# Kernel optimization log

Measured on AMD Instinct MI355X. Metric: run time of the kernel, lower is better.

The kernel has to match this reference:

```python
import jax, jax.numpy as jnp
import numpy as np
import math

EMBED_DIM = 1024
NUM_HEADS = 16
HEAD_DIM = EMBED_DIM // NUM_HEADS
ROPE_BASE = 10000.0


def _rope_cache(seq_len, dim, dtype=jnp.float32):
    inv_freq = 1.0 / (ROPE_BASE ** (jnp.arange(0, dim, 2, dtype=jnp.float32) / dim))
    t = jnp.arange(seq_len, dtype=jnp.float32)
    freqs = t[:, None] * inv_freq[None, :]          # [S, D/2]
    emb = jnp.concatenate([freqs, freqs], axis=-1)  # [S, D]
    return jnp.cos(emb).astype(dtype), jnp.sin(emb).astype(dtype)


def _rotate_half(x):
    x1, x2 = jnp.split(x, 2, axis=-1)
    return jnp.concatenate([-x2, x1], axis=-1)


def setup_inputs() -> dict:
    key = jax.random.key(0)
    ks = jax.random.split(key, 12)
    B, S, E = 2, 2048, EMBED_DIM
    s = 1.0 / math.sqrt(E)
    inp = {
        "query": jax.random.normal(ks[0], (B, S, E), jnp.float32),
        "key": jax.random.normal(ks[1], (B, S, E), jnp.float32),
        "value": jax.random.normal(ks[2], (B, S, E), jnp.float32),
        "Wq": jax.random.normal(ks[3], (E, E), jnp.float32) * s,
        "bq": jnp.zeros((E,), jnp.float32),
        "Wk": jax.random.normal(ks[4], (E, E), jnp.float32) * s,
        "bk": jnp.zeros((E,), jnp.float32),
        "Wv": jax.random.normal(ks[5], (E, E), jnp.float32) * s,
        "bv": jnp.zeros((E,), jnp.float32),
        "Wo": jax.random.normal(ks[6], (E, E), jnp.float32) * s,
        "bo": jnp.zeros((E,), jnp.float32),
    }
    return inp


def reference(query, key, value, Wq, bq, Wk, bk, Wv, bv, Wo, bo):
    B, S, E = query.shape
    H, D = NUM_HEADS, HEAD_DIM

    def proj(x, W, b):  # torch Linear: x @ W.T + b -> [B,H,S,D]
        return (x @ W.T + b).reshape(B, -1, H, D).transpose(0, 2, 1, 3)

    q = proj(query, Wq, bq)
    k = proj(key, Wk, bk)
    v = proj(value, Wv, bv)

    cos, sin = _rope_cache(S, D, q.dtype)  # [S, D]
    cos = cos[None, None]                  # [1,1,S,D]
    sin = sin[None, None]
    q = q * cos + _rotate_half(q) * sin
    k = k * cos + _rotate_half(k) * sin

    scale = 1.0 / math.sqrt(D)
    scores = jnp.einsum("bhsd,bhtd->bhst", q, k) * scale  # [B,H,S,S]
    causal = jnp.triu(jnp.ones((S, S), bool), k=1)
    scores = jnp.where(causal[None, None], -jnp.inf, scores)
    attn = jax.nn.softmax(scores, axis=-1)
    out = jnp.einsum("bhst,bhtd->bhsd", attn, v)           # [B,H,S,D]
    out = out.transpose(0, 2, 1, 3).reshape(B, S, E)
    return out @ Wo.T + bo
```

## Files before the change

### kernel.cpp

```cpp
#include <hip/hip_runtime.h>
#include <math.h>

typedef unsigned short u16;
typedef __attribute__((ext_vector_type(4))) float f32x4;
typedef __attribute__((ext_vector_type(8))) short bf16x8;

#define SEQ   2048
#define EMB   1024
#define NH    16
#define HD    64
#define MROWS 4096

__device__ __forceinline__ u16 f2b(float f) {
    unsigned u = __float_as_uint(f);
    u += 0x7fff + ((u >> 16) & 1);
    return (u16)(u >> 16);
}
__device__ __forceinline__ unsigned pack_bf16x2(float a, float b) {
    unsigned ua = __float_as_uint(a) + 0x8000u;
    unsigned ub = __float_as_uint(b) + 0x8000u;
    return __builtin_amdgcn_perm(ub, ua, 0x07060302u);
}
__device__ __forceinline__ void gld16(const u16* g, const u16* l) {
    __builtin_amdgcn_global_load_lds((const __attribute__((address_space(1))) void*)g,
                                     (__attribute__((address_space(3))) void*)l, 16, 0, 0);
}

__global__ void k_f2b3(const float* __restrict__ s0, const float* __restrict__ s1,
                       const float* __restrict__ s2, u16* d0, u16* d1, u16* d2, int n8) {
    const float* src = (blockIdx.z == 0) ? s0 : (blockIdx.z == 1 ? s1 : s2);
    u16* dst = (blockIdx.z == 0) ? d0 : (blockIdx.z == 1 ? d1 : d2);
    int i = blockIdx.x * blockDim.x + threadIdx.x;
    if (i >= n8) return;
    const float4* s4 = (const float4*)src;
    float4 a = s4[i * 2], b = s4[i * 2 + 1];
    union { u16 u[8]; uint4 v; } o;
    o.u[0] = f2b(a.x); o.u[1] = f2b(a.y); o.u[2] = f2b(a.z); o.u[3] = f2b(a.w);
    o.u[4] = f2b(b.x); o.u[5] = f2b(b.y); o.u[6] = f2b(b.z); o.u[7] = f2b(b.w);
    ((uint4*)dst)[i] = o.v;
}
__global__ void k_f2b4(const float* __restrict__ s0, const float* __restrict__ s1,
                       const float* __restrict__ s2, const float* __restrict__ s3,
                       u16* d0, u16* d1, u16* d2, u16* d3, int n8) {
    const float* src = (blockIdx.z == 0) ? s0 : (blockIdx.z == 1 ? s1 : (blockIdx.z == 2 ? s2 : s3));
    u16* dst = (blockIdx.z == 0) ? d0 : (blockIdx.z == 1 ? d1 : (blockIdx.z == 2 ? d2 : d3));
    int i = blockIdx.x * blockDim.x + threadIdx.x;
    if (i >= n8) return;
    const float4* s4 = (const float4*)src;
    float4 a = s4[i * 2], b = s4[i * 2 + 1];
    union { u16 u[8]; uint4 v; } o;
    o.u[0] = f2b(a.x); o.u[1] = f2b(a.y); o.u[2] = f2b(a.z); o.u[3] = f2b(a.w);
    o.u[4] = f2b(b.x); o.u[5] = f2b(b.y); o.u[6] = f2b(b.z); o.u[7] = f2b(b.w);
    ((uint4*)dst)[i] = o.v;
}

struct GemmArgs {
    const u16* A; const u16* Bw; const float* bias; u16* Cb;
};

__global__ __launch_bounds__(256) void k_gemm_qkv(GemmArgs g0, GemmArgs g1, GemmArgs g2) {
    GemmArgs g = (blockIdx.z == 0) ? g0 : (blockIdx.z == 1 ? g1 : g2);
    __shared__ union {
        u16 s[2][8192];
        u16 tr[4][4608];
    } sh;

    int tid = threadIdx.x;
    int wave = tid >> 6, lane = tid & 63, quad = lane >> 4, l16 = lane & 15;
    int wm = wave >> 1, wn = wave & 1;
    int m0 = blockIdx.y * 128, n0 = blockIdx.x * 128;
    const int K = EMB;

    auto stage = [&](int k0, u16* buf) {
#pragma unroll
        for (int pp = 0; pp < 4; pp++) {
            int slot = pp * 256 + tid;
            int p = slot & 3;
            const u16* gsrc;
            if (pp < 2) {
                int row = slot >> 2;
                int c = p ^ (row & 3);
                gsrc = g.A + (size_t)(m0 + row) * K + k0 + c * 8;
            } else {
                int row = (slot >> 2) - 128;
                int c = p ^ (row & 3);
                gsrc = g.Bw + (size_t)(n0 + row) * K + k0 + c * 8;
            }
            gld16(gsrc, buf + slot * 8);
        }
    };

    f32x4 acc[4][4];
#pragma unroll
    for (int i = 0; i < 4; i++)
#pragma unroll
        for (int j = 0; j < 4; j++) acc[i][j] = (f32x4){0.f, 0.f, 0.f, 0.f};

    int nk = K >> 5;
    stage(0, sh.s[0]);
    for (int ks = 0; ks < nk; ks++) {
        __syncthreads();
        if (ks + 1 < nk) stage((ks + 1) << 5, sh.s[(ks + 1) & 1]);
        const u16* Ab = sh.s[ks & 1];
        const u16* Bb = Ab + 4096;
        bf16x8 af[4], bfr[4];
#pragma unroll
        for (int i = 0; i < 4; i++) {
            int row = wm * 64 + i * 16 + l16;
            af[i] = *(const bf16x8*)&Ab[row * 32 + (quad ^ (row & 3)) * 8];
        }
#pragma unroll
        for (int j = 0; j < 4; j++) {
            int row = wn * 64 + j * 16 + l16;
            bfr[j] = *(const bf16x8*)&Bb[row * 32 + (quad ^ (row & 3)) * 8];
        }
#pragma unroll
        for (int i = 0; i < 4; i++)
#pragma unroll
            for (int j = 0; j < 4; j++)
                acc[i][j] = __builtin_amdgcn_mfma_f32_16x16x32_bf16(af[i], bfr[j], acc[i][j], 0, 0, 0);
    }

    if (blockIdx.z < 2) {
        float qscale = (blockIdx.z == 0) ? 0.18033688011112042f : 1.0f;
#pragma unroll
        for (int j = 0; j < 2; j++) {
            int col1 = n0 + wn * 64 + j * 16 + l16;
            int dd1 = col1 & 63;
            int h = col1 >> 6;
            float inv = __expf(-(float)dd1 * 0.28782313662425575f);
            float b1 = g.bias[col1], b2 = g.bias[col1 + 32];
#pragma unroll
            for (int i = 0; i < 4; i++)
#pragma unroll
                for (int r = 0; r < 4; r++) {
                    int row = m0 + wm * 64 + i * 16 + quad * 4 + r;
                    int b = row >> 11, s = row & (SEQ - 1);
                    float sn, cs;
                    __sincosf((float)s * inv, &sn, &cs);
                    float x1 = acc[i][j][r] + b1;
                    float x2 = acc[i][j + 2][r] + b2;
                    size_t base = ((size_t)(b * NH + h) * SEQ + s) << 6;
                    g.Cb[base + dd1]      = f2b((x1 * cs - x2 * sn) * qscale);
                    g.Cb[base + dd1 + 32] = f2b((x2 * cs + x1 * sn) * qscale);
                }
        }
    } else {
        __syncthreads();
        u16* tr = sh.tr[wave];
        int h = (n0 >> 6) + wn;
        int b = m0 >> 11;
        int s0 = (m0 & (SEQ - 1)) + wm * 64;
#pragma unroll
        for (int j = 0; j < 4; j++) {
            float bv = g.bias[n0 + wn * 64 + j * 16 + l16];
#pragma unroll
            for (int i = 0; i < 4; i++) {
                uint2 pk;
                pk.x = pack_bf16x2(acc[i][j][0] + bv, acc[i][j][1] + bv);
                pk.y = pack_bf16x2(acc[i][j][2] + bv, acc[i][j][3] + bv);
                *(uint2*)&tr[(j * 16 + l16) * 72 + i * 16 + quad * 4] = pk;
            }
        }
        u16* dst = g.Cb + (((size_t)(b * NH + h) * HD) * SEQ) + s0;
#pragma unroll
        for (int ps = 0; ps < 8; ps++) {
            int d = ps * 8 + (lane >> 3);
            int sl = (lane & 7) * 8;
            uint4 v = *(const uint4*)&tr[d * 72 + sl];
            *(uint4*)&dst[(size_t)d * SEQ + sl] = v;
        }
    }
}

__global__ __launch_bounds__(256) void k_gemm_o(const u16* __restrict__ A,
                                                const u16* __restrict__ Bw,
                                                const float* __restrict__ bias,
                                                float* __restrict__ C) {
    __shared__ u16 sb[2][6144];
    int tid = threadIdx.x;
    int w = tid >> 6, lane = tid & 63, quad = lane >> 4, l16 = lane & 15;
    int m0 = blockIdx.y * 64, n0 = blockIdx.x * 128;
    const int K = EMB;

    auto stage = [&](int k0, u16* buf) {
#pragma unroll
        for (int pp = 0; pp < 3; pp++) {
            int slot = pp * 256 + tid;
            if (slot < 256) {
                int row = slot >> 2, p = slot & 3;
                int c = p ^ (row & 3);
                gld16(A + (size_t)(m0 + row) * K + k0 + c * 8, buf + slot * 8);
            } else {
                int s2 = slot - 256;
                int row = s2 >> 2, p = s2 & 3;
                int c = p ^ (row & 3);
                gld16(Bw + (size_t)(n0 + row) * K + k0 + c * 8, buf + 2048 + s2 * 8);
            }
        }
    };

    f32x4 acc[4][2];
#pragma unroll
    for (int i = 0; i < 4; i++)
#pragma unroll
        for (int j = 0; j < 2; j++) acc[i][j] = (f32x4){0.f, 0.f, 0.f, 0.f};

    int nk = K >> 5;
    stage(0, sb[0]);
    for (int ks = 0; ks < nk; ks++) {
        __syncthreads();
        if (ks + 1 < nk) stage((ks + 1) << 5, sb[(ks + 1) & 1]);
        const u16* Ab = sb[ks & 1];
        const u16* Bb = Ab + 2048;
        bf16x8 af[4], bf[2];
#pragma unroll
        for (int i = 0; i < 4; i++) {
            int row = i * 16 + l16;
            af[i] = *(const bf16x8*)&Ab[row * 32 + (quad ^ (row & 3)) * 8];
        }
#pragma unroll
        for (int j = 0; j < 2; j++) {
            int row = w * 32 + j * 16 + l16;
            bf[j] = *(const bf16x8*)&Bb[row * 32 + (quad ^ (row & 3)) * 8];
        }
#pragma unroll
        for (int i = 0; i < 4; i++)
#pragma unroll
            for (int j = 0; j < 2; j++)
                acc[i][j] = __builtin_amdgcn_mfma_f32_16x16x32_bf16(af[i], bf[j], acc[i][j], 0, 0, 0);
    }

#pragma unroll
    for (int i = 0; i < 4; i++)
#pragma unroll
        for (int r = 0; r < 4; r++) {
            int row = m0 + i * 16 + quad * 4 + r;
#pragma unroll
            for (int j = 0; j < 2; j++) {
                int col = n0 + w * 32 + j * 16 + l16;
                C[(size_t)row * EMB + col] = acc[i][j][r] + bias[col];
            }
        }
}

__global__ __launch_bounds__(256, 2) void k_attn(const u16* __restrict__ Q,
                                                 const u16* __restrict__ K,
                                                 const u16* __restrict__ Vt,
                                                 u16* __restrict__ O) {
    __shared__ u16 sbuf[2][8192];
    __shared__ u16 Pl[4][2048];
    int tid = threadIdx.x;
    int w = tid >> 6, lane = tid & 63, quad = lane >> 4, l16 = lane & 15;
    int bh = blockIdx.x & 31;
    int qt = 15 - (blockIdx.x >> 5);
    int q0w = qt * 128 + w * 32;

    const u16* Qb = Q + (size_t)bh * SEQ * HD;
    const u16* Kb = K + (size_t)bh * SEQ * HD;
    const u16* Vb = Vt + (size_t)bh * HD * SEQ;
    u16* pl = Pl[w];

    auto stage = [&](int t0, u16* buf) {
#pragma unroll
        for (int pp = 0; pp < 4; pp++) {
            int slot = pp * 256 + tid;
            int r = (slot >> 3) & 63;
            int p = slot & 7;
            int c = p ^ (r & 7);
            const u16* gsrc = (pp < 2) ? Kb + (size_t)(t0 + r) * HD + c * 8
                                       : Vb + (size_t)r * SEQ + t0 + c * 8;
            gld16(gsrc, buf + slot * 8);
        }
    };

    bf16x8 bq[2][2];
#pragma unroll
    for (int g = 0; g < 2; g++) {
        size_t base = (size_t)(q0w + g * 16 + l16) * HD + quad * 8;
        bq[g][0] = *(const bf16x8*)&Qb[base];
        bq[g][1] = *(const bf16x8*)&Qb[base + 32];
    }

    f32x4 o2[2][4];
#pragma unroll
    for (int g = 0; g < 2; g++)
#pragma unroll
        for (int jd = 0; jd < 4; jd++) o2[g][jd] = (f32x4){0.f, 0.f, 0.f, 0.f};
    float l_p[2] = {0.f, 0.f};

    int niter = 2 * qt + 2;
    stage(0, sbuf[0]);
    for (int it = 0; it < niter; ++it) {
        __syncthreads();
        if (it + 1 < niter) stage((it + 1) * 64, sbuf[(it + 1) & 1]);
        const u16* Kl = sbuf[it & 1];
        const u16* Vl = Kl + 4096;
        int t0 = it * 64;

        bf16x8 kf[4][2], vf[4][2];
#pragma unroll
        for (int mt = 0; mt < 4; mt++) {
            int row = mt * 16 + l16;
            kf[mt][0] = *(const bf16x8*)&Kl[row * 64 + (quad ^ (row & 7)) * 8];
            kf[mt][1] = *(const bf16x8*)&Kl[row * 64 + ((quad + 4) ^ (row & 7)) * 8];
            vf[mt][0] = *(const bf16x8*)&Vl[row * 64 + (quad ^ (row & 7)) * 8];
            vf[mt][1] = *(const bf16x8*)&Vl[row * 64 + ((quad + 4) ^ (row & 7)) * 8];
        }

#pragma unroll
        for (int g = 0; g < 2; g++) {
            int qmin = q0w + g * 16;
            if (t0 > qmin + 15) continue;

            f32x4 sc[4];
#pragma unroll
            for (int mt = 0; mt < 4; mt++) {
                sc[mt] = (f32x4){0.f, 0.f, 0.f, 0.f};
                sc[mt] = __builtin_amdgcn_mfma_f32_16x16x32_bf16(kf[mt][0], bq[g][0], sc[mt], 0, 0, 0);
                sc[mt] = __builtin_amdgcn_mfma_f32_16x16x32_bf16(kf[mt][1], bq[g][1], sc[mt], 0, 0, 0);
            }

            if (t0 + 63 > qmin) {
                int q = qmin + l16;
#pragma unroll
                for (int mt = 0; mt < 4; mt++)
#pragma unroll
                    for (int r = 0; r < 4; r++) {
                        int t = t0 + mt * 16 + quad * 4 + r;
                        if (t > q) sc[mt][r] = -INFINITY;
                    }
            }

            float rs = 0.f;
#pragma unroll
            for (int mt = 0; mt < 4; mt++)
#pragma unroll
                for (int r = 0; r < 4; r++) {
                    float p = __builtin_amdgcn_exp2f(sc[mt][r] - 64.f);
                    sc[mt][r] = p;
                    rs += p;
                }
            l_p[g] += rs;

            u16* plg = pl + g * 1024;
#pragma unroll
            for (int mt = 0; mt < 4; mt++) {
                uint2 pk;
                pk.x = pack_bf16x2(sc[mt][0], sc[mt][1]);
                pk.y = pack_bf16x2(sc[mt][2], sc[mt][3]);
                int chunk = 2 * mt + (quad >> 1);
                *(uint2*)&plg[l16 * 64 + (chunk ^ (l16 & 7)) * 8 + (quad & 1) * 4] = pk;
            }

            bf16x8 pb0 = *(const bf16x8*)&plg[l16 * 64 + (quad ^ (l16 & 7)) * 8];
            bf16x8 pb1 = *(const bf16x8*)&plg[l16 * 64 + ((quad + 4) ^ (l16 & 7)) * 8];

#pragma unroll
            for (int jd = 0; jd < 4; jd++) {
                o2[g][jd] = __builtin_amdgcn_mfma_f32_16x16x32_bf16(vf[jd][0], pb0, o2[g][jd], 0, 0, 0);
                o2[g][jd] = __builtin_amdgcn_mfma_f32_16x16x32_bf16(vf[jd][1], pb1, o2[g][jd], 0, 0, 0);
            }
        }
    }

    int b = bh >> 4, h = bh & (NH - 1);
#pragma unroll
    for (int g = 0; g < 2; g++) {
        float l = l_p[g];
        l += __shfl_xor(l, 16, 64);
        l += __shfl_xor(l, 32, 64);
        float inv = 1.f / l;
#pragma unroll
        for (int jd = 0; jd < 4; jd++) {
            uint2 pk;
            pk.x = pack_bf16x2(o2[g][jd][0] * inv, o2[g][jd][1] * inv);
            pk.y = pack_bf16x2(o2[g][jd][2] * inv, o2[g][jd][3] * inv);
            *(uint2*)&pl[l16 * 72 + jd * 16 + quad * 4] = pk;
        }
        int row = lane >> 2, dc = (lane & 3) * 16;
        uint4 d0 = *(const uint4*)&pl[row * 72 + dc];
        uint4 d1 = *(const uint4*)&pl[row * 72 + dc + 8];
        int q = q0w + g * 16 + row;
        size_t addr = (size_t)(b * SEQ + q) * EMB + h * HD + dc;
        *(uint4*)&O[addr] = d0;
        *(uint4*)&O[addr + 8] = d1;
    }
}

extern "C" void kernel_launch(void* const* d_in, const int* in_sizes, int n_in,
                              void* d_out, int out_size, void* d_ws, size_t ws_size,
                              hipStream_t stream) {
    const float* query = (const float*)d_in[0];
    const float* key_  = (const float*)d_in[1];
    const float* value = (const float*)d_in[2];
    const float* Wq = (const float*)d_in[3];
    const float* bq = (const float*)d_in[4];
    const float* Wk = (const float*)d_in[5];
    const float* bk = (const float*)d_in[6];
    const float* Wv = (const float*)d_in[7];
    const float* bv = (const float*)d_in[8];
    const float* Wo = (const float*)d_in[9];
    const float* bo = (const float*)d_in[10];
    float* out = (float*)d_out;

    char* ws = (char*)d_ws;
    const size_t MB = 1u << 20;
    u16* xq  = (u16*)(ws + 0 * MB);
    u16* xk  = (u16*)(ws + 8 * MB);
    u16* xv  = (u16*)(ws + 16 * MB);
    u16* wqb = (u16*)(ws + 24 * MB);
    u16* wkb = (u16*)(ws + 26 * MB);
    u16* wvb = (u16*)(ws + 28 * MB);
    u16* wob = (u16*)(ws + 30 * MB);
    u16* Qp  = (u16*)(ws + 32 * MB);
    u16* Kp  = (u16*)(ws + 40 * MB);
    u16* Vt  = (u16*)(ws + 48 * MB);
    u16* Ab  = xk;

    const int NX = MROWS * EMB;
    const int NW = EMB * EMB;

    k_f2b3<<<dim3(NX / (256 * 8), 1, 3), 256, 0, stream>>>(query, key_, value, xq, xk, xv, NX / 8);
    k_f2b4<<<dim3(NW / (256 * 8), 1, 4), 256, 0, stream>>>(Wq, Wk, Wv, Wo, wqb, wkb, wvb, wob, NW / 8);

    GemmArgs gq = { xq, wqb, bq, Qp };
    GemmArgs gk = { xk, wkb, bk, Kp };
    GemmArgs gv = { xv, wvb, bv, Vt };
    k_gemm_qkv<<<dim3(EMB / 128, MROWS / 128, 3), 256, 0, stream>>>(gq, gk, gv);

    k_attn<<<512, 256, 0, stream>>>(Qp, Kp, Vt, Ab);

    k_gemm_o<<<dim3(EMB / 128, MROWS / 64), 256, 0, stream>>>(Ab, wob, bo, out);
}
```

Before: 225.3 us.

## Merge conversion launches, remap GEMM block order, swizzle V-transpose shared buffer

After: 216.5 us. -3.9%, faster.

```diff
diff --git a/kernel.cpp b/kernel.cpp
--- a/kernel.cpp
+++ b/kernel.cpp
@@ -26,31 +26,27 @@
                                      (__attribute__((address_space(3))) void*)l, 16, 0, 0);
 }
 
-__global__ void k_f2b3(const float* __restrict__ s0, const float* __restrict__ s1,
-                       const float* __restrict__ s2, u16* d0, u16* d1, u16* d2, int n8) {
-    const float* src = (blockIdx.z == 0) ? s0 : (blockIdx.z == 1 ? s1 : s2);
-    u16* dst = (blockIdx.z == 0) ? d0 : (blockIdx.z == 1 ? d1 : d2);
-    int i = blockIdx.x * blockDim.x + threadIdx.x;
-    if (i >= n8) return;
+struct F2BArgs { const float* s[7]; u16* d[7]; };
+
+__global__ void k_f2b(F2BArgs a) {
+    int id = blockIdx.x;
+    const float* src; u16* dst; int base;
+    if (id < 6144) {
+        int z = id >> 11;
+        src = a.s[z]; dst = a.d[z];
+        base = (id & 2047) << 8;
+    } else {
+        int r = id - 6144;
+        int z = 3 + (r >> 9);
+        src = a.s[z]; dst = a.d[z];
+        base = (r & 511) << 8;
+    }
+    int i = base + threadIdx.x;
     const float4* s4 = (const float4*)src;
-    float4 a = s4[i * 2], b = s4[i * 2 + 1];
+    float4 x = s4[i * 2], y = s4[i * 2 + 1];
     union { u16 u[8]; uint4 v; } o;
-    o.u[0] = f2b(a.x); o.u[1] = f2b(a.y); o.u[2] = f2b(a.z); o.u[3] = f2b(a.w);
-    o.u[4] = f2b(b.x); o.u[5] = f2b(b.y); o.u[6] = f2b(b.z); o.u[7] = f2b(b.w);
-    ((uint4*)dst)[i] = o.v;
-}
-__global__ void k_f2b4(const float* __restrict__ s0, const float* __restrict__ s1,
-                       const float* __restrict__ s2, const float* __restrict__ s3,
-                       u16* d0, u16* d1, u16* d2, u16* d3, int n8) {
-    const float* src = (blockIdx.z == 0) ? s0 : (blockIdx.z == 1 ? s1 : (blockIdx.z == 2 ? s2 : s3));
-    u16* dst = (blockIdx.z == 0) ? d0 : (blockIdx.z == 1 ? d1 : (blockIdx.z == 2 ? d2 : d3));
-    int i = blockIdx.x * blockDim.x + threadIdx.x;
-    if (i >= n8) return;
-    const float4* s4 = (const float4*)src;
-    float4 a = s4[i * 2], b = s4[i * 2 + 1];
-    union { u16 u[8]; uint4 v; } o;
-    o.u[0] = f2b(a.x); o.u[1] = f2b(a.y); o.u[2] = f2b(a.z); o.u[3] = f2b(a.w);
-    o.u[4] = f2b(b.x); o.u[5] = f2b(b.y); o.u[6] = f2b(b.z); o.u[7] = f2b(b.w);
+    o.u[0] = f2b(x.x); o.u[1] = f2b(x.y); o.u[2] = f2b(x.z); o.u[3] = f2b(x.w);
+    o.u[4] = f2b(y.x); o.u[5] = f2b(y.y); o.u[6] = f2b(y.z); o.u[7] = f2b(y.w);
     ((uint4*)dst)[i] = o.v;
 }
 
@@ -59,16 +55,19 @@
 };
 
 __global__ __launch_bounds__(256) void k_gemm_qkv(GemmArgs g0, GemmArgs g1, GemmArgs g2) {
-    GemmArgs g = (blockIdx.z == 0) ? g0 : (blockIdx.z == 1 ? g1 : g2);
-    __shared__ union {
-        u16 s[2][8192];
-        u16 tr[4][4608];
-    } sh;
+    __shared__ u16 sbuf[2][8192];
+
+    int id = blockIdx.x;
+    int x = id / 96;
+    int rem = id % 96;
+    int z = rem >> 5;
+    int y = rem & 31;
+    GemmArgs g = (z == 0) ? g0 : (z == 1 ? g1 : g2);
 
     int tid = threadIdx.x;
     int wave = tid >> 6, lane = tid & 63, quad = lane >> 4, l16 = lane & 15;
     int wm = wave >> 1, wn = wave & 1;
-    int m0 = blockIdx.y * 128, n0 = blockIdx.x * 128;
+    int m0 = y * 128, n0 = x * 128;
     const int K = EMB;
 
     auto stage = [&](int k0, u16* buf) {
@@ -97,11 +96,11 @@
         for (int j = 0; j < 4; j++) acc[i][j] = (f32x4){0.f, 0.f, 0.f, 0.f};
 
     int nk = K >> 5;
-    stage(0, sh.s[0]);
+    stage(0, sbuf[0]);
     for (int ks = 0; ks < nk; ks++) {
         __syncthreads();
-        if (ks + 1 < nk) stage((ks + 1) << 5, sh.s[(ks + 1) & 1]);
-        const u16* Ab = sh.s[ks & 1];
+        if (ks + 1 < nk) stage((ks + 1) << 5, sbuf[(ks + 1) & 1]);
+        const u16* Ab = sbuf[ks & 1];
         const u16* Bb = Ab + 4096;
         bf16x8 af[4], bfr[4];
 #pragma unroll
@@ -121,8 +120,8 @@
                 acc[i][j] = __builtin_amdgcn_mfma_f32_16x16x32_bf16(af[i], bfr[j], acc[i][j], 0, 0, 0);
     }
 
-    if (blockIdx.z < 2) {
-        float qscale = (blockIdx.z == 0) ? 0.18033688011112042f : 1.0f;
+    if (z < 2) {
+        float qscale = (z == 0) ? 0.18033688011112042f : 1.0f;
 #pragma unroll
         for (int j = 0; j < 2; j++) {
             int col1 = n0 + wn * 64 + j * 16 + l16;
@@ -147,7 +146,7 @@
         }
     } else {
         __syncthreads();
-        u16* tr = sh.tr[wave];
+        u16* tr = &sbuf[0][0] + wave * 4096;
         int h = (n0 >> 6) + wn;
         int b = m0 >> 11;
         int s0 = (m0 & (SEQ - 1)) + wm * 64;
@@ -159,16 +158,18 @@
                 uint2 pk;
                 pk.x = pack_bf16x2(acc[i][j][0] + bv, acc[i][j][1] + bv);
                 pk.y = pack_bf16x2(acc[i][j][2] + bv, acc[i][j][3] + bv);
-                *(uint2*)&tr[(j * 16 + l16) * 72 + i * 16 + quad * 4] = pk;
+                int row = j * 16 + l16;
+                int c4 = i * 4 + quad;
+                *(uint2*)&tr[row * 64 + ((c4 ^ (row & 14)) << 2)] = pk;
             }
         }
         u16* dst = g.Cb + (((size_t)(b * NH + h) * HD) * SEQ) + s0;
 #pragma unroll
         for (int ps = 0; ps < 8; ps++) {
             int d = ps * 8 + (lane >> 3);
-            int sl = (lane & 7) * 8;
-            uint4 v = *(const uint4*)&tr[d * 72 + sl];
-            *(uint4*)&dst[(size_t)d * SEQ + sl] = v;
+            int c4 = (lane & 7) * 2;
+            uint4 v = *(const uint4*)&tr[d * 64 + ((c4 ^ (d & 14)) << 2)];
+            *(uint4*)&dst[(size_t)d * SEQ + c4 * 4] = v;
         }
     }
 }
@@ -180,7 +181,8 @@
     __shared__ u16 sb[2][6144];
     int tid = threadIdx.x;
     int w = tid >> 6, lane = tid & 63, quad = lane >> 4, l16 = lane & 15;
-    int m0 = blockIdx.y * 64, n0 = blockIdx.x * 128;
+    int y = blockIdx.x & 63, x = blockIdx.x >> 6;
+    int m0 = y * 64, n0 = x * 128;
     const int K = EMB;
 
     auto stage = [&](int k0, u16* buf) {
@@ -418,18 +420,19 @@
     u16* Vt  = (u16*)(ws + 48 * MB);
     u16* Ab  = xk;
 
-    const int NX = MROWS * EMB;
-    const int NW = EMB * EMB;
-
-    k_f2b3<<<dim3(NX / (256 * 8), 1, 3), 256, 0, stream>>>(query, key_, value, xq, xk, xv, NX / 8);
-    k_f2b4<<<dim3(NW / (256 * 8), 1, 4), 256, 0, stream>>>(Wq, Wk, Wv, Wo, wqb, wkb, wvb, wob, NW / 8);
+    F2BArgs fa;
+    fa.s[0] = query; fa.s[1] = key_; fa.s[2] = value;
+    fa.s[3] = Wq; fa.s[4] = Wk; fa.s[5] = Wv; fa.s[6] = Wo;
+    fa.d[0] = xq; fa.d[1] = xk; fa.d[2] = xv;
+    fa.d[3] = wqb; fa.d[4] = wkb; fa.d[5] = wvb; fa.d[6] = wob;
+    k_f2b<<<8192, 256, 0, stream>>>(fa);
 
     GemmArgs gq = { xq, wqb, bq, Qp };
     GemmArgs gk = { xk, wkb, bk, Kp };
     GemmArgs gv = { xv, wvb, bv, Vt };
-    k_gemm_qkv<<<dim3(EMB / 128, MROWS / 128, 3), 256, 0, stream>>>(gq, gk, gv);
+    k_gemm_qkv<<<768, 256, 0, stream>>>(gq, gk, gv);
 
     k_attn<<<512, 256, 0, stream>>>(Qp, Kp, Vt, Ab);
 
-    k_gemm_o<<<dim3(EMB / 128, MROWS / 64), 256, 0, stream>>>(Ab, wob, bo, out);
-}
+    k_gemm_o<<<512, 256, 0, stream>>>(Ab, wob, bo, out);
+}
```
